# Optimization experiments

Measured on AMD Instinct MI355X. Metric: run time of the kernel, lower is better.

Reference implementation:

```python
import jax, jax.numpy as jnp
import numpy as np

S, B, D = 2048, 2, 768
H = 12
R = 64  # adapter bottleneck


def setup_inputs() -> dict:
    key = jax.random.key(0)
    ks = jax.random.split(key, 16)
    d = {
        'query': jax.random.normal(ks[0], (S, B, D), jnp.float32),
        'key':   jax.random.normal(ks[1], (S, B, D), jnp.float32),
        'value': jax.random.normal(ks[2], (S, B, D), jnp.float32),
        'in_proj_w': jax.random.normal(ks[3], (3 * D, D), jnp.float32) * (D ** -0.5),
        'in_proj_b': jax.random.normal(ks[4], (3 * D,), jnp.float32) * 0.02,
        'ssf_scale_1': 1.0 + 0.02 * jax.random.normal(ks[5], (3 * D,), jnp.float32),
        'ssf_shift_1': 0.02 * jax.random.normal(ks[6], (3 * D,), jnp.float32),
        'lora1_down_w': jax.random.normal(ks[7], (R, D), jnp.float32) * (D ** -0.5),
        'lora1_down_b': jnp.zeros((R,), jnp.float32),
        'lora1_up_w': jax.random.normal(ks[8], (3 * D, R), jnp.float32) * 0.02,
        'lora1_up_b': jnp.zeros((3 * D,), jnp.float32),
        'lora1_scale': jnp.ones((1,), jnp.float32),
        'out_w': jax.random.normal(ks[9], (D, D), jnp.float32) * (D ** -0.5),
        'out_b': jnp.zeros((D,), jnp.float32),
        'ssf_scale_2': 1.0 + 0.02 * jax.random.normal(ks[10], (D,), jnp.float32),
        'ssf_shift_2': 0.02 * jax.random.normal(ks[11], (D,), jnp.float32),
        'lora2_down_w': jax.random.normal(ks[12], (R, D), jnp.float32) * (D ** -0.5),
        'lora2_down_b': jnp.zeros((R,), jnp.float32),
        'lora2_up_w': jax.random.normal(ks[13], (D, R), jnp.float32) * 0.02,
        'lora2_up_b': jnp.zeros((D,), jnp.float32),
        'lora2_scale': jnp.ones((1,), jnp.float32),
        'num_heads': H,
    }
    return d


def _adapter(x, dw, db, uw, ub, scale):
    # down -> relu -> up -> * scalar (dropout inactive, add_residual=False)
    h = jax.nn.relu(jnp.einsum('sbd,rd->sbr', x, dw) + db)
    return (jnp.einsum('sbr,er->sbe', h, uw) + ub) * scale[0]


def reference(query, key, value, in_proj_w, in_proj_b, ssf_scale_1, ssf_shift_1,
              lora1_down_w, lora1_down_b, lora1_up_w, lora1_up_b, lora1_scale,
              out_w, out_b, ssf_scale_2, ssf_shift_2,
              lora2_down_w, lora2_down_b, lora2_up_w, lora2_up_b, lora2_scale,
              num_heads):
    tgt, bsz, d = query.shape
    hd = d // num_heads
    scaling = hd ** -0.5
    # fused QKV projection + SSF scale/shift + LoRA adapter on query
    qkv = jnp.einsum('sbd,ed->sbe', query, in_proj_w) + in_proj_b
    qkv = qkv * ssf_scale_1 + ssf_shift_1
    qkv = qkv + _adapter(query, lora1_down_w, lora1_down_b, lora1_up_w, lora1_up_b, lora1_scale)
    q, k, v = jnp.split(qkv, 3, axis=-1)
    q = q * scaling
    # [S,B,D] -> [B*H, S, hd]
    def to_heads(t):
        return t.reshape(tgt, bsz * num_heads, hd).transpose(1, 0, 2)
    q, k, v = to_heads(q), to_heads(k), to_heads(v)
    attn = jax.nn.softmax(jnp.einsum('nqh,nkh->nqk', q, k), axis=-1)
    out = jnp.einsum('nqk,nkh->nqh', attn, v)  # [B*H, S, hd]
    out = out.transpose(1, 0, 2).reshape(tgt, bsz, d)
    # lora2 on pre-projection attn output
    ad2 = _adapter(out, lora2_down_w, lora2_down_b, lora2_up_w, lora2_up_b, lora2_scale)
    o = jnp.einsum('sbd,ed->sbe', out, out_w) + out_b
    o = o * ssf_scale_2 + ssf_shift_2
    return o + ad2
```

## Files before the change

kernel.cpp:

```cpp
#include <hip/hip_runtime.h>
#include <stdint.h>

typedef float f32x4 __attribute__((ext_vector_type(4)));
typedef _Float16 f16x8 __attribute__((ext_vector_type(8)));
typedef _Float16 f16x4 __attribute__((ext_vector_type(4)));
typedef unsigned int u32x2 __attribute__((ext_vector_type(2)));

#define MFMAH(a, b, c)  __builtin_amdgcn_mfma_f32_16x16x32_f16(a, b, c, 0, 0, 0)
#define MFMAH16(a, b, c) __builtin_amdgcn_mfma_f32_16x16x16f16(a, b, c, 0, 0, 0)

#define GLOAD16(gp, lp) __builtin_amdgcn_global_load_lds( \
    (__attribute__((address_space(1))) void*)(void*)(gp), \
    (__attribute__((address_space(3))) void*)(void*)(lp), 16, 0, 0)

#define QSCALE (0.125f * 1.44269504f)
#define SMOFF 8.0f

static __device__ inline f32x4 zero4() { f32x4 z; z[0]=0.f; z[1]=0.f; z[2]=0.f; z[3]=0.f; return z; }

static __device__ inline unsigned int pk2(float a, float b) {
  return __builtin_bit_cast(unsigned int, __builtin_amdgcn_cvt_pkrtz(a, b));
}

__global__ void k_pre(const float* __restrict__ s0, const float* __restrict__ s1,
                      const float* __restrict__ s2, const float* __restrict__ s3,
                      const float* __restrict__ s4,
                      _Float16* __restrict__ d0, _Float16* __restrict__ d1,
                      _Float16* __restrict__ d2, _Float16* __restrict__ d3,
                      _Float16* __restrict__ d4,
                      int n0, int n1, int n2, int n3, int n4,
                      const float* __restrict__ uw1, const float* __restrict__ sc1,
                      const float* __restrict__ lsc1, _Float16* __restrict__ up1,
                      const float* __restrict__ uw2, const float* __restrict__ sc2,
                      const float* __restrict__ lsc2, _Float16* __restrict__ up2,
                      const float* __restrict__ b1, const float* __restrict__ sh1,
                      const float* __restrict__ ub1, float* __restrict__ c1,
                      const float* __restrict__ b2, const float* __restrict__ sh2,
                      const float* __restrict__ ub2, float* __restrict__ c2) {
  int gid = blockIdx.x*blockDim.x + threadIdx.x;
  if (gid < 2304*64) up1[gid] = (_Float16)(uw1[gid] * lsc1[0] / sc1[gid >> 6]);
  if (gid < 768*64)  up2[gid] = (_Float16)(uw2[gid] * lsc2[0] / sc2[gid >> 6]);
  if (gid < 2304)    c1[gid] = sc1[gid]*b1[gid] + sh1[gid] + lsc1[0]*ub1[gid];
  if (gid < 768)     c2[gid] = sc2[gid]*b2[gid] + sh2[gid] + lsc2[0]*ub2[gid];
  int total = n0 + n1 + n2 + n3 + n4;
  for (int i = gid; i < total; i += gridDim.x*blockDim.x) {
    const float* src; _Float16* dst; int j = i;
    if (j < n0) { src = s0; dst = d0; }
    else { j -= n0;
      if (j < n1) { src = s1; dst = d1; }
      else { j -= n1;
        if (j < n2) { src = s2; dst = d2; }
        else { j -= n2;
          if (j < n3) { src = s3; dst = d3; }
          else { j -= n3; src = s4; dst = d4; }
        }
      }
    }
    float4 v = ((const float4*)src)[j];
    f16x4 o;
    o[0] = (_Float16)v.x; o[1] = (_Float16)v.y; o[2] = (_Float16)v.z; o[3] = (_Float16)v.w;
    ((f16x4*)dst)[j] = o;
  }
}

__global__ __launch_bounds__(256) void k_lora_h(const _Float16* __restrict__ A,
    const _Float16* __restrict__ Dw, const float* __restrict__ db, _Float16* __restrict__ H) {
  const int wave = threadIdx.x >> 6, lane = threadIdx.x & 63;
  const int g = lane >> 4, li = lane & 15;
  const int rowbase = blockIdx.x * 16;
  __shared__ f32x4 part[4][4][64];
  f32x4 acc[4];
  #pragma unroll
  for (int nt = 0; nt < 4; nt++) acc[nt] = zero4();
  const int kbase = wave * 192;
  for (int k0 = 0; k0 < 192; k0 += 32) {
    f16x8 a = *(const f16x8*)(A + (size_t)(rowbase + li)*768 + kbase + k0 + g*8);
    #pragma unroll
    for (int nt = 0; nt < 4; nt++) {
      f16x8 b = *(const f16x8*)(Dw + (size_t)(nt*16 + li)*768 + kbase + k0 + g*8);
      acc[nt] = MFMAH(a, b, acc[nt]);
    }
  }
  #pragma unroll
  for (int nt = 0; nt < 4; nt++) part[wave][nt][lane] = acc[nt];
  __syncthreads();
  f32x4 s = part[0][wave][lane];
  #pragma unroll
  for (int p = 1; p < 4; p++) {
    f32x4 t = part[p][wave][lane];
    s[0] += t[0]; s[1] += t[1]; s[2] += t[2]; s[3] += t[3];
  }
  int r = wave*16 + li;
  float bias = db[r];
  #pragma unroll
  for (int j = 0; j < 4; j++) {
    float v = s[j] + bias;
    H[(size_t)(rowbase + g*4 + j)*64 + r] = (_Float16)fmaxf(v, 0.f);
  }
}

template<int EPI>
__global__ __launch_bounds__(256, 3) void k_gemm(
    const _Float16* __restrict__ A, const _Float16* __restrict__ B,
    const _Float16* __restrict__ Ha, const _Float16* __restrict__ Up,
    const float* __restrict__ Sc, const float* __restrict__ Cst,
    float* __restrict__ Cout, _Float16* __restrict__ qh,
    _Float16* __restrict__ kh, _Float16* __restrict__ vT) {
  __shared__ _Float16 lsA[2][4096];
  __shared__ _Float16 lsB[2][3072];
  const int tid = threadIdx.x;
  const int wave = tid >> 6, lane = tid & 63;
  const int g = lane >> 4, li = lane & 15;
  const int wr = wave >> 1, wc = wave & 1;
  const int rb = blockIdx.x * 128, cb = blockIdx.y * 96;

  f32x4 acc[4][3];
  #pragma unroll
  for (int m = 0; m < 4; m++)
    #pragma unroll
    for (int n = 0; n < 3; n++) acc[m][n] = zero4();

  auto stage = [&](int buf, int k0) {
    #pragma unroll
    for (int c = 0; c < 2; c++) {
      int p = c*256 + tid;
      int r = p >> 2, cp = p & 3;
      int cc = (cp - (r >> 1)) & 3;
      GLOAD16(A + (size_t)(rb + r)*768 + k0 + cc*8, &lsA[buf][(c*256 + wave*64)*8]);
      if (c == 0 || tid < 128)
        GLOAD16(B + (size_t)(cb + r)*768 + k0 + cc*8, &lsB[buf][(c*256 + wave*64)*8]);
    }
  };

  stage(0, 0);
  __syncthreads();
  int cur = 0;
  for (int t = 0; t < 24; t++) {
    if (t + 1 < 24) stage(cur ^ 1, (t + 1) * 32);
    f16x8 ah[4], bh[3];
    #pragma unroll
    for (int m = 0; m < 4; m++) {
      int row = wr*64 + m*16 + li;
      int cp = (g + (row >> 1)) & 3;
      ah[m] = *(const f16x8*)(&lsA[cur][row*32 + cp*8]);
    }
    #pragma unroll
    for (int n = 0; n < 3; n++) {
      int row = wc*48 + n*16 + li;
      int cp = (g + (row >> 1)) & 3;
      bh[n] = *(const f16x8*)(&lsB[cur][row*32 + cp*8]);
    }
    __builtin_amdgcn_s_setprio(1);
    #pragma unroll
    for (int m = 0; m < 4; m++)
      #pragma unroll
      for (int n = 0; n < 3; n++)
        acc[m][n] = MFMAH(ah[m], bh[n], acc[m][n]);
    __builtin_amdgcn_s_setprio(0);
    __syncthreads();
    cur ^= 1;
  }

  _Float16* l0a = &lsA[0][0];
  _Float16* l0b = &lsB[0][0];
  #pragma unroll
  for (int c = 0; c < 4; c++) {
    int p = c*256 + tid;
    int r = p >> 3, cp = p & 7;
    int cc = (cp - r) & 7;
    GLOAD16(Ha + (size_t)(rb + r)*64 + cc*8, l0a + (c*256 + wave*64)*8);
    if (c < 3)
      GLOAD16(Up + (size_t)(cb + r)*64 + cc*8, l0b + (c*256 + wave*64)*8);
  }
  __syncthreads();
  #pragma unroll
  for (int s = 0; s < 2; s++) {
    f16x8 ha[4], ub[3];
    #pragma unroll
    for (int m = 0; m < 4; m++) {
      int row = wr*64 + m*16 + li;
      int cp = ((s*4 + g) + row) & 7;
      ha[m] = *(const f16x8*)(l0a + row*64 + cp*8);
    }
    #pragma unroll
    for (int n = 0; n < 3; n++) {
      int row = wc*48 + n*16 + li;
      int cp = ((s*4 + g) + row) & 7;
      ub[n] = *(const f16x8*)(l0b + row*64 + cp*8);
    }
    #pragma unroll
    for (int m = 0; m < 4; m++)
      #pragma unroll
      for (int n = 0; n < 3; n++)
        acc[m][n] = MFMAH(ha[m], ub[n], acc[m][n]);
  }

  #pragma unroll
  for (int n = 0; n < 3; n++) {
    int col = cb + wc*48 + n*16 + li;
    float sc = Sc[col], ct = Cst[col];
    #pragma unroll
    for (int m = 0; m < 4; m++) {
      #pragma unroll
      for (int j = 0; j < 4; j++) {
        int row = rb + wr*64 + m*16 + g*4 + j;
        float v = sc * acc[m][n][j] + ct;
        if (EPI == 0) {
          Cout[(size_t)row*768 + col] = v;
        } else {
          int sect = col / 768;
          int eh = col - sect*768;
          int hh = eh >> 6, hd = eh & 63;
          int si = row >> 1, bb = row & 1;
          int nh = bb*12 + hh;
          if (sect == 0)      qh[((size_t)nh*2048 + si)*64 + hd] = (_Float16)(v * QSCALE);
          else if (sect == 1) kh[((size_t)nh*2048 + si)*64 + hd] = (_Float16)v;
          else                vT[((size_t)nh*64 + hd)*2048 + si] = (_Float16)v;
        }
      }
    }
  }
}

__global__ __launch_bounds__(256, 3) void k_attn(const _Float16* __restrict__ qh,
    const _Float16* __restrict__ kh, const _Float16* __restrict__ vT,
    _Float16* __restrict__ outf) {
  const int wave = threadIdx.x >> 6, lane = threadIdx.x & 63;
  const int g = lane >> 4, li = lane & 15;
  const int head = blockIdx.x;
  const int q0 = blockIdx.y*64;
  const _Float16* Qb = qh + (size_t)head*2048*64;
  const _Float16* Kb = kh + (size_t)head*2048*64;
  const _Float16* Vb = vT + (size_t)head*64*2048;
  __shared__ char smem[36864];
  _Float16* Kt = (_Float16*)smem;
  _Float16* Vt = (_Float16*)(smem + 16384);

  auto stage = [&](int buf, int kb) {
    #pragma unroll
    for (int c = 0; c < 2; c++) {
      int idx = c*256 + wave*64 + lane;
      int r = idx >> 3, cp = idx & 7;
      int csrc = cp ^ (r & 7);
      GLOAD16(Kb + (size_t)(kb + r)*64 + csrc*8, Kt + buf*4096 + (c*256 + wave*64)*8);
      GLOAD16(Vb + (size_t)r*2048 + kb + csrc*8, Vt + buf*4096 + (c*256 + wave*64)*8);
    }
  };

  f16x8 qf[4][2];
  #pragma unroll
  for (int ct = 0; ct < 4; ct++)
    #pragma unroll
    for (int dw = 0; dw < 2; dw++)
      qf[ct][dw] = *(const f16x8*)(Qb + (size_t)(q0 + 16*ct + li)*64 + dw*32 + g*8);

  f32x4 o[4][4];
  #pragma unroll
  for (int dt = 0; dt < 4; dt++)
    #pragma unroll
    for (int qt = 0; qt < 4; qt++) o[dt][qt] = zero4();
  float sj[4] = {0.f, 0.f, 0.f, 0.f};
  const int sw = li & 7;

  stage(0, 0);
  __syncthreads();
  int cur = 0;
  for (int t = 0; t < 32; t++) {
    if (t + 1 < 32) stage(cur ^ 1, (t + 1) * 64);
    const _Float16* Kl = Kt + cur*4096;
    const _Float16* Vl = Vt + cur*4096;
    const int krow = 16*wave + li;
    f16x8 kf0 = *(const f16x8*)(Kl + krow*64 + (g ^ sw)*8);
    f16x8 kf1 = *(const f16x8*)(Kl + krow*64 + ((4 + g) ^ sw)*8);
    f32x4 c[4];
    __builtin_amdgcn_s_setprio(1);
    #pragma unroll
    for (int ct = 0; ct < 4; ct++) {
      c[ct][0] = -SMOFF; c[ct][1] = -SMOFF; c[ct][2] = -SMOFF; c[ct][3] = -SMOFF;
      c[ct] = MFMAH(kf0, qf[ct][0], c[ct]);
      c[ct] = MFMAH(kf1, qf[ct][1], c[ct]);
    }
    __builtin_amdgcn_s_setprio(0);
    f16x4 pf[4];
    #pragma unroll
    for (int ct = 0; ct < 4; ct++) {
      float p0 = __builtin_amdgcn_exp2f(c[ct][0]);
      float p1 = __builtin_amdgcn_exp2f(c[ct][1]);
      float p2 = __builtin_amdgcn_exp2f(c[ct][2]);
      float p3 = __builtin_amdgcn_exp2f(c[ct][3]);
      sj[ct] += (p0 + p1) + (p2 + p3);
      u32x2 pk; pk[0] = pk2(p0, p1); pk[1] = pk2(p2, p3);
      pf[ct] = __builtin_bit_cast(f16x4, pk);
    }
    __builtin_amdgcn_s_setprio(1);
    #pragma unroll
    for (int dt = 0; dt < 4; dt++) {
      const int drow = 16*dt + li;
      const _Float16* va = Vl + drow*64 + (((2*wave + (g >> 1)) ^ sw)*8) + 4*(g & 1);
      f16x4 vf = *(const f16x4*)va;
      #pragma unroll
      for (int qt = 0; qt < 4; qt++)
        o[dt][qt] = MFMAH16(vf, pf[qt], o[dt][qt]);
    }
    __builtin_amdgcn_s_setprio(0);
    __syncthreads();
    cur ^= 1;
  }

  _Float16* part = (_Float16*)smem;
  float* lrp = (float*)(smem + 32768);
  #pragma unroll
  for (int dt = 0; dt < 4; dt++)
    #pragma unroll
    for (int qt = 0; qt < 4; qt++) {
      u32x2 pw;
      pw[0] = pk2(o[dt][qt][0], o[dt][qt][1]);
      pw[1] = pk2(o[dt][qt][2], o[dt][qt][3]);
      *(u32x2*)(part + ((wave*16 + dt*4 + qt)*64 + lane)*4) = pw;
    }
  #pragma unroll
  for (int ct = 0; ct < 4; ct++) {
    float a = sj[ct];
    a += __shfl_xor(a, 16);
    a += __shfl_xor(a, 32);
    lrp[(wave*4 + ct)*64 + lane] = a;
  }
  __syncthreads();
  const int bb = head / 12, hh = head % 12;
  #pragma unroll
  for (int qt = 0; qt < 4; qt++) {
    float lr = lrp[qt*64 + lane] + lrp[(4 + qt)*64 + lane]
             + lrp[(8 + qt)*64 + lane] + lrp[(12 + qt)*64 + lane];
    float inv = 1.f / lr;
    float s0 = 0.f, s1 = 0.f, s2 = 0.f, s3 = 0.f;
    #pragma unroll
    for (int p = 0; p < 4; p++) {
      f16x4 pv = *(const f16x4*)(part + ((p*16 + wave*4 + qt)*64 + lane)*4);
      s0 += (float)pv[0]; s1 += (float)pv[1]; s2 += (float)pv[2]; s3 += (float)pv[3];
    }
    const int si = q0 + 16*qt + li;
    f16x4 ov;
    ov[0] = (_Float16)(s0 * inv); ov[1] = (_Float16)(s1 * inv);
    ov[2] = (_Float16)(s2 * inv); ov[3] = (_Float16)(s3 * inv);
    *(f16x4*)(&outf[((size_t)si*2 + bb)*768 + hh*64 + 16*wave + 4*g]) = ov;
  }
}

extern "C" void kernel_launch(void* const* d_in, const int* in_sizes, int n_in,
                              void* d_out, int out_size, void* d_ws, size_t ws_size,
                              hipStream_t stream) {
  (void)in_sizes; (void)n_in; (void)out_size; (void)ws_size;
  const float* query = (const float*)d_in[0];
  const float* w1   = (const float*)d_in[3];
  const float* b1   = (const float*)d_in[4];
  const float* s1   = (const float*)d_in[5];
  const float* sh1  = (const float*)d_in[6];
  const float* dw1  = (const float*)d_in[7];
  const float* db1  = (const float*)d_in[8];
  const float* uw1  = (const float*)d_in[9];
  const float* ub1  = (const float*)d_in[10];
  const float* lsc1 = (const float*)d_in[11];
  const float* w2   = (const float*)d_in[12];
  const float* b2   = (const float*)d_in[13];
  const float* s2   = (const float*)d_in[14];
  const float* sh2  = (const float*)d_in[15];
  const float* dw2  = (const float*)d_in[16];
  const float* db2  = (const float*)d_in[17];
  const float* uw2  = (const float*)d_in[18];
  const float* ub2  = (const float*)d_in[19];
  const float* lsc2 = (const float*)d_in[20];
  float* out = (float*)d_out;

  char* ws = (char*)d_ws;
  size_t off = 0;
  auto alloc = [&](size_t bytes) -> char* {
    char* p = ws + off; off += (bytes + 255) & ~(size_t)255; return p;
  };
  typedef _Float16 F16;
  F16* qf16 = (F16*)alloc((size_t)4096*768*2);
  F16* w1f  = (F16*)alloc((size_t)2304*768*2);
  F16* w2f  = (F16*)alloc((size_t)768*768*2);
  F16* d1f  = (F16*)alloc((size_t)64*768*2);
  F16* d2f  = (F16*)alloc((size_t)64*768*2);
  F16* up1p = (F16*)alloc((size_t)2304*64*2);
  F16* up2p = (F16*)alloc((size_t)768*64*2);
  float* c1 = (float*)alloc((size_t)2304*4);
  float* c2 = (float*)alloc((size_t)768*4);
  F16* h1   = (F16*)alloc((size_t)4096*64*2);
  F16* h2   = (F16*)alloc((size_t)4096*64*2);
  F16* qhd  = (F16*)alloc((size_t)24*2048*64*2);
  F16* khd  = (F16*)alloc((size_t)24*2048*64*2);
  F16* vTd  = (F16*)alloc((size_t)24*64*2048*2);
  F16* of16 = (F16*)alloc((size_t)4096*768*2);

  k_pre<<<2048, 256, 0, stream>>>(query, w1, w2, dw1, dw2,
                                  qf16, w1f, w2f, d1f, d2f,
                                  4096*768/4, 2304*768/4, 768*768/4,
                                  64*768/4, 64*768/4,
                                  uw1, s1, lsc1, up1p, uw2, s2, lsc2, up2p,
                                  b1, sh1, ub1, c1, b2, sh2, ub2, c2);
  k_lora_h<<<256, 256, 0, stream>>>(qf16, d1f, db1, h1);
  k_gemm<1><<<dim3(32, 24), 256, 0, stream>>>(qf16, w1f, h1, up1p, s1, c1,
                                              nullptr, qhd, khd, vTd);
  k_attn<<<dim3(24, 32), 256, 0, stream>>>(qhd, khd, vTd, of16);
  k_lora_h<<<256, 256, 0, stream>>>(of16, d2f, db2, h2);
  k_gemm<0><<<dim3(32, 8), 256, 0, stream>>>(of16, w2f, h2, up2p, s2, c2,
                                             out, nullptr, nullptr, nullptr);
}
```

Before: 104.5 us.

## Load K/V fragments directly from global into registers, dropping LDS staging

The attention loop stops staging K and V tiles through shared memory with async global-to-LDS copies and block-wide barriers. Each wave now loads its own K and V fragments straight from global memory into registers, double-buffered in registers across pairs of iterations. This removes LDS traffic and per-iteration __syncthreads. The cost is more registers and uncoalesced, strided global loads, especially the 8-byte V reads with a 2048-element stride, which lean on the cache.

```diff
diff --git a/kernel.cpp b/kernel.cpp
--- a/kernel.cpp
+++ b/kernel.cpp
@@ -233,20 +233,9 @@
   const _Float16* Kb = kh + (size_t)head*2048*64;
   const _Float16* Vb = vT + (size_t)head*64*2048;
   __shared__ char smem[36864];
-  _Float16* Kt = (_Float16*)smem;
-  _Float16* Vt = (_Float16*)(smem + 16384);
-
-  auto stage = [&](int buf, int kb) {
-    #pragma unroll
-    for (int c = 0; c < 2; c++) {
-      int idx = c*256 + wave*64 + lane;
-      int r = idx >> 3, cp = idx & 7;
-      int csrc = cp ^ (r & 7);
-      GLOAD16(Kb + (size_t)(kb + r)*64 + csrc*8, Kt + buf*4096 + (c*256 + wave*64)*8);
-      GLOAD16(Vb + (size_t)r*2048 + kb + csrc*8, Vt + buf*4096 + (c*256 + wave*64)*8);
-    }
-  };
-
+
+  const _Float16* kp = Kb + (size_t)(16*wave + li)*64 + g*8;
+  const _Float16* vp0 = Vb + (size_t)(li)*2048 + 16*wave + 4*g;
   f16x8 qf[4][2];
   #pragma unroll
   for (int ct = 0; ct < 4; ct++)
@@ -260,18 +249,15 @@
     #pragma unroll
     for (int qt = 0; qt < 4; qt++) o[dt][qt] = zero4();
   float sj[4] = {0.f, 0.f, 0.f, 0.f};
-  const int sw = li & 7;
-
-  stage(0, 0);
-  __syncthreads();
-  int cur = 0;
-  for (int t = 0; t < 32; t++) {
-    if (t + 1 < 32) stage(cur ^ 1, (t + 1) * 64);
-    const _Float16* Kl = Kt + cur*4096;
-    const _Float16* Vl = Vt + cur*4096;
-    const int krow = 16*wave + li;
-    f16x8 kf0 = *(const f16x8*)(Kl + krow*64 + (g ^ sw)*8);
-    f16x8 kf1 = *(const f16x8*)(Kl + krow*64 + ((4 + g) ^ sw)*8);
+
+  f16x8 kA0, kA1, kB0, kB1;
+  f16x4 vA[4], vB[4];
+  kA0 = *(const f16x8*)(kp);
+  kA1 = *(const f16x8*)(kp + 32);
+  #pragma unroll
+  for (int dt = 0; dt < 4; dt++) vA[dt] = *(const f16x4*)(vp0 + (size_t)dt*16*2048);
+
+  auto compute = [&](const f16x8& kf0, const f16x8& kf1, const f16x4* vf) {
     f32x4 c[4];
     __builtin_amdgcn_s_setprio(1);
     #pragma unroll
@@ -294,17 +280,32 @@
     }
     __builtin_amdgcn_s_setprio(1);
     #pragma unroll
-    for (int dt = 0; dt < 4; dt++) {
-      const int drow = 16*dt + li;
-      const _Float16* va = Vl + drow*64 + (((2*wave + (g >> 1)) ^ sw)*8) + 4*(g & 1);
-      f16x4 vf = *(const f16x4*)va;
+    for (int dt = 0; dt < 4; dt++)
       #pragma unroll
       for (int qt = 0; qt < 4; qt++)
-        o[dt][qt] = MFMAH16(vf, pf[qt], o[dt][qt]);
-    }
+        o[dt][qt] = MFMAH16(vf[dt], pf[qt], o[dt][qt]);
     __builtin_amdgcn_s_setprio(0);
-    __syncthreads();
-    cur ^= 1;
+  };
+
+  for (int t = 0; t < 32; t += 2) {
+    {
+      const _Float16* kq = kp + (size_t)(t + 1)*64*64;
+      const _Float16* vq = vp0 + (t + 1)*64;
+      kB0 = *(const f16x8*)(kq);
+      kB1 = *(const f16x8*)(kq + 32);
+      #pragma unroll
+      for (int dt = 0; dt < 4; dt++) vB[dt] = *(const f16x4*)(vq + (size_t)dt*16*2048);
+    }
+    compute(kA0, kA1, vA);
+    if (t + 2 < 32) {
+      const _Float16* kq = kp + (size_t)(t + 2)*64*64;
+      const _Float16* vq = vp0 + (t + 2)*64;
+      kA0 = *(const f16x8*)(kq);
+      kA1 = *(const f16x8*)(kq + 32);
+      #pragma unroll
+      for (int dt = 0; dt < 4; dt++) vA[dt] = *(const f16x4*)(vq + (size_t)dt*16*2048);
+    }
+    compute(kB0, kB1, vB);
   }
 
   _Float16* part = (_Float16*)smem;
```

Result: slower. 138.8 us (+32.8%).

## Load K fragments directly from global into registers, stage only V in LDS

Applied to the files above, without the earlier changes.

The attention loop no longer stages K tiles through shared memory. Each wave now loads its own K fragment straight from global memory into registers, one tile ahead, and alternates between two named register sets with the loop unrolled by two. V is still staged in LDS with double buffering. This cuts LDS traffic and the LDS reads for K, but each K load now has global latency that must be hidden behind one tile of compute, and it gives up the swizzled LDS access pattern for K.

```diff
diff --git a/kernel.cpp b/kernel.cpp
--- a/kernel.cpp
+++ b/kernel.cpp
@@ -233,19 +233,19 @@
   const _Float16* Kb = kh + (size_t)head*2048*64;
   const _Float16* Vb = vT + (size_t)head*64*2048;
   __shared__ char smem[36864];
-  _Float16* Kt = (_Float16*)smem;
-  _Float16* Vt = (_Float16*)(smem + 16384);
-
-  auto stage = [&](int buf, int kb) {
+  _Float16* Vt = (_Float16*)smem;
+
+  auto stageV = [&](int buf, int kb) {
     #pragma unroll
     for (int c = 0; c < 2; c++) {
       int idx = c*256 + wave*64 + lane;
       int r = idx >> 3, cp = idx & 7;
       int csrc = cp ^ (r & 7);
-      GLOAD16(Kb + (size_t)(kb + r)*64 + csrc*8, Kt + buf*4096 + (c*256 + wave*64)*8);
       GLOAD16(Vb + (size_t)r*2048 + kb + csrc*8, Vt + buf*4096 + (c*256 + wave*64)*8);
     }
   };
+
+  const _Float16* kp = Kb + (size_t)(16*wave + li)*64 + g*8;
 
   f16x8 qf[4][2];
   #pragma unroll
@@ -262,16 +262,7 @@
   float sj[4] = {0.f, 0.f, 0.f, 0.f};
   const int sw = li & 7;
 
-  stage(0, 0);
-  __syncthreads();
-  int cur = 0;
-  for (int t = 0; t < 32; t++) {
-    if (t + 1 < 32) stage(cur ^ 1, (t + 1) * 64);
-    const _Float16* Kl = Kt + cur*4096;
-    const _Float16* Vl = Vt + cur*4096;
-    const int krow = 16*wave + li;
-    f16x8 kf0 = *(const f16x8*)(Kl + krow*64 + (g ^ sw)*8);
-    f16x8 kf1 = *(const f16x8*)(Kl + krow*64 + ((4 + g) ^ sw)*8);
+  auto compute = [&](const f16x8& kf0, const f16x8& kf1, const _Float16* Vl) {
     f32x4 c[4];
     __builtin_amdgcn_s_setprio(1);
     #pragma unroll
@@ -303,8 +294,26 @@
         o[dt][qt] = MFMAH16(vf, pf[qt], o[dt][qt]);
     }
     __builtin_amdgcn_s_setprio(0);
+  };
+
+  f16x8 kA0, kA1, kB0, kB1;
+  kA0 = *(const f16x8*)(kp);
+  kA1 = *(const f16x8*)(kp + 32);
+  stageV(0, 0);
+  __syncthreads();
+  for (int t = 0; t < 32; t += 2) {
+    stageV(1, (t + 1) * 64);
+    kB0 = *(const f16x8*)(kp + (t + 1)*4096);
+    kB1 = *(const f16x8*)(kp + (t + 1)*4096 + 32);
+    compute(kA0, kA1, Vt);
     __syncthreads();
-    cur ^= 1;
+    if (t + 2 < 32) {
+      stageV(0, (t + 2) * 64);
+      kA0 = *(const f16x8*)(kp + (t + 2)*4096);
+      kA1 = *(const f16x8*)(kp + (t + 2)*4096 + 32);
+    }
+    compute(kB0, kB1, Vt + 4096);
+    __syncthreads();
   }
 
   _Float16* part = (_Float16*)smem;
```

Result: slower. 106.6 us (+2.1%).
